# Kernel optimization log

Measured on AMD Instinct MI355X. Metric: run time of the kernel, lower is better.

Reference implementation:

```python
import jax, jax.numpy as jnp
import numpy as np

B, S, D, H = 4, 2048, 512, 4
HD = D // H
EPS = 1e-5


def layer_norm(x, gamma, beta):
    mu = jnp.mean(x, axis=-1, keepdims=True)
    var = jnp.mean(jnp.square(x - mu), axis=-1, keepdims=True)
    return (x - mu) * jax.lax.rsqrt(var + EPS) * gamma + beta


def setup_inputs() -> dict:
    key = jax.random.key(0)
    ks = jax.random.split(key, 16)
    s_in = 1.0 / np.sqrt(D)
    s_ex = 1.0 / np.sqrt(2 * D)
    return {
        "input_states": jax.random.normal(ks[0], (B, S, D), jnp.float32),
        "positions": jax.random.normal(ks[1], (B, S, 3), jnp.float32),
        "W_expand": jax.random.uniform(ks[2], (D, 2 * D), jnp.float32, -s_in, s_in),
        "b_expand": jax.random.uniform(ks[3], (2 * D,), jnp.float32, -s_in, s_in),
        "W_squeeze": jax.random.uniform(ks[4], (2 * D, D), jnp.float32, -s_ex, s_ex),
        "b_squeeze": jax.random.uniform(ks[5], (D,), jnp.float32, -s_ex, s_ex),
        "gamma": jnp.ones((D,), jnp.float32),
        "beta": jnp.zeros((D,), jnp.float32),
        "Wq": jax.random.uniform(ks[6], (D, D), jnp.float32, -s_in, s_in),
        "bq": jax.random.uniform(ks[7], (D,), jnp.float32, -s_in, s_in),
        "Wk": jax.random.uniform(ks[8], (D, D), jnp.float32, -s_in, s_in),
        "bk": jax.random.uniform(ks[9], (D,), jnp.float32, -s_in, s_in),
        "Wv": jax.random.uniform(ks[10], (D, D), jnp.float32, -s_in, s_in),
        "bv": jax.random.uniform(ks[11], (D,), jnp.float32, -s_in, s_in),
        "alpha": jnp.float32(0.1),
    }


def reference(input_states, positions, W_expand, b_expand, W_squeeze, b_squeeze,
              gamma, beta, Wq, bq, Wk, bk, Wv, bv, alpha):
    # FFN (expand -> relu -> squeeze) + residual + LayerNorm
    h = jax.nn.relu(input_states @ W_expand + b_expand)
    squeezed = h @ W_squeeze + b_squeeze
    se = layer_norm(input_states + squeezed, gamma, beta)

    # q/k/v projections, split heads: [B,H,S,HD]
    q = (se @ Wq + bq).reshape(B, S, H, HD).transpose(0, 2, 1, 3)
    k = (se @ Wk + bk).reshape(B, S, H, HD).transpose(0, 2, 1, 3)
    v = (se @ Wv + bv).reshape(B, S, H, HD).transpose(0, 2, 1, 3)

    scores = jnp.einsum('bhid,bhjd->bhij', q, k) / np.sqrt(HD)

    # squared pairwise distance bias: ||pi||^2 + ||pj||^2 - 2 pi.pj, broadcast over heads
    sq = jnp.sum(positions * positions, axis=-1)  # [B,S]
    dist2 = sq[:, :, None] + sq[:, None, :] - 2.0 * jnp.einsum('bic,bjc->bij', positions, positions)
    dist2 = jnp.maximum(dist2, 0.0)
    scores = scores - alpha * dist2[:, None, :, :]

    w = jax.nn.softmax(scores, axis=-1)
    ctx = jnp.einsum('bhij,bhjd->bhid', w, v)
    ctx = ctx.transpose(0, 2, 1, 3).reshape(B, S, D)

    # same LayerNorm params reused (self.norm applied twice in original)
    return layer_norm(se + ctx, gamma, beta)
```

## Files before the change

### kernel.cpp

```cpp
#include <hip/hip_runtime.h>

typedef __bf16 bf16_t;
typedef __attribute__((ext_vector_type(8))) __bf16 bf16x8;
typedef __attribute__((ext_vector_type(4))) __bf16 bf16x4;
typedef __attribute__((ext_vector_type(4))) float f32x4;

constexpr int Bc = 4, Sc = 2048, Dc = 512, Hc = 4, HDc = 128;
constexpr int Mrows = Bc * Sc;

__device__ inline void gl2lds(const void* g, void* l) {
  __builtin_amdgcn_global_load_lds(
      (__attribute__((address_space(1))) void*)g,
      (__attribute__((address_space(3))) void*)l, 16, 0, 0);
}

__global__ __launch_bounds__(256) void prep_k(
    const float* __restrict__ X, bf16_t* __restrict__ xb,
    const float* __restrict__ We, bf16_t* __restrict__ wtE,
    const float* __restrict__ Ws, bf16_t* __restrict__ wtS,
    const float* __restrict__ Wq, const float* __restrict__ Wk,
    const float* __restrict__ Wv, bf16_t* __restrict__ wtQKV) {
  const int bid = blockIdx.x;
  if (bid < 2048) {
    const long i = ((long)bid * 256 + threadIdx.x) * 8;
    const float4 a = *(const float4*)(X + i);
    const float4 c = *(const float4*)(X + i + 4);
    bf16x8 o;
    o[0] = (bf16_t)a.x; o[1] = (bf16_t)a.y; o[2] = (bf16_t)a.z; o[3] = (bf16_t)a.w;
    o[4] = (bf16_t)c.x; o[5] = (bf16_t)c.y; o[6] = (bf16_t)c.z; o[7] = (bf16_t)c.w;
    *(bf16x8*)(xb + i) = o;
    return;
  }
  __shared__ float tile[32][33];
  const float* src; bf16_t* dst; int K, N, local;
  if (bid < 2560)      { src = We; dst = wtE; K = 512;  N = 1024; local = bid - 2048; }
  else if (bid < 3072) { src = Ws; dst = wtS; K = 1024; N = 512;  local = bid - 2560; }
  else if (bid < 3328) { src = Wq; dst = wtQKV;          K = 512; N = 512; local = bid - 3072; }
  else if (bid < 3584) { src = Wk; dst = wtQKV + 262144; K = 512; N = 512; local = bid - 3328; }
  else                 { src = Wv; dst = wtQKV + 524288; K = 512; N = 512; local = bid - 3584; }
  const int nb = N / 32;
  const int n0 = (local % nb) * 32, k0 = (local / nb) * 32;
  const int tx = threadIdx.x & 31, ty = threadIdx.x >> 5;
#pragma unroll
  for (int i = 0; i < 4; i++)
    tile[ty + i * 8][tx] = src[(long)(k0 + ty + i * 8) * N + n0 + tx];
  __syncthreads();
#pragma unroll
  for (int i = 0; i < 4; i++)
    dst[(long)(n0 + ty + i * 8) * K + k0 + tx] = (bf16_t)tile[tx][ty + i * 8];
}

__global__ __launch_bounds__(256) void pospack_k(const float* __restrict__ pos,
                                                 const float* __restrict__ alphap,
                                                 float* __restrict__ pos2) {
  const float aL = alphap[0] * 1.4426950408889634f;
  const int i = blockIdx.x * 256 + threadIdx.x;
  const float x = pos[(long)i * 3], y = pos[(long)i * 3 + 1], z = pos[(long)i * 3 + 2];
  float4 o; o.x = x; o.y = y; o.z = z; o.w = -aL * (x * x + y * y + z * z);
  *(float4*)(pos2 + (long)i * 4) = o;
}

template <int OMODE>
__global__ __launch_bounds__(256, 3) void gemm128_k(
    const bf16_t* __restrict__ A, const bf16_t* __restrict__ Bt,
    const float* __restrict__ bias0, const float* __restrict__ bias1,
    const float* __restrict__ bias2, void* __restrict__ out0,
    void* __restrict__ out1, void* __restrict__ out2, int N, int K) {
  __shared__ bf16_t As[128 * 64];
  __shared__ bf16_t Bs[128 * 64];
  const int t = threadIdx.x;
  const int n0 = blockIdx.x * 128, m0 = blockIdx.y * 128;
  const int lane = t & 63, wave = t >> 6;
  const int quad = lane >> 4, ln = lane & 15;
  const int wm = wave >> 1, wn = wave & 1;
  const int srow = wave * 32 + (lane >> 3);
  const int sgrp = lane & 7;
  const bf16_t* aseg = A + (long)(m0 + srow) * K + sgrp * 8;
  const bf16_t* bseg = Bt + (long)(n0 + srow) * K + sgrp * 8;
  bf16_t* asl = &As[(wave * 32) * 64];
  bf16_t* bsl = &Bs[(wave * 32) * 64];
  f32x4 acc[4][4] = {};
  for (int k0 = 0; k0 < K; k0 += 64) {
#pragma unroll
    for (int i = 0; i < 4; i++) {
      gl2lds(aseg + (long)i * 8 * K + k0, asl + i * 8 * 64);
      gl2lds(bseg + (long)i * 8 * K + k0, bsl + i * 8 * 64);
    }
    __syncthreads();
#pragma unroll
    for (int kc = 0; kc < 2; kc++) {
      bf16x8 af[4], bfr[4];
#pragma unroll
      for (int mt = 0; mt < 4; mt++)
        af[mt] = *(const bf16x8*)&As[(wm * 64 + mt * 16 + ln) * 64 + kc * 32 + quad * 8];
#pragma unroll
      for (int nt = 0; nt < 4; nt++)
        bfr[nt] = *(const bf16x8*)&Bs[(wn * 64 + nt * 16 + ln) * 64 + kc * 32 + quad * 8];
#pragma unroll
      for (int mt = 0; mt < 4; mt++)
#pragma unroll
        for (int nt = 0; nt < 4; nt++)
          acc[mt][nt] = __builtin_amdgcn_mfma_f32_16x16x32_bf16(af[mt], bfr[nt],
                                                                acc[mt][nt], 0, 0, 0);
    }
    __syncthreads();
  }
#pragma unroll
  for (int nt = 0; nt < 4; nt++) {
    const int gcol = n0 + wn * 64 + nt * 16 + ln;
    if constexpr (OMODE == 0 || OMODE == 1) {
      const float bv = bias0[gcol];
      bf16_t* o = (bf16_t*)out0;
#pragma unroll
      for (int mt = 0; mt < 4; mt++)
#pragma unroll
        for (int r = 0; r < 4; r++) {
          const int grow = m0 + wm * 64 + mt * 16 + quad * 4 + r;
          float vv = acc[mt][nt][r] + bv;
          if constexpr (OMODE == 0) vv = vv > 0.f ? vv : 0.f;
          o[(long)grow * N + gcol] = (bf16_t)vv;
        }
    } else {
      const int which = gcol >> 9, n = gcol & 511;
      const int hh = n >> 7, hd = n & 127;
      const float bv = (which == 0 ? bias0 : which == 1 ? bias1 : bias2)[n];
      bf16_t* o = (bf16_t*)(which == 0 ? out0 : which == 1 ? out1 : out2);
#pragma unroll
      for (int mt = 0; mt < 4; mt++)
#pragma unroll
        for (int r = 0; r < 4; r++) {
          const int grow = m0 + wm * 64 + mt * 16 + quad * 4 + r;
          const int b = grow >> 11, s = grow & 2047;
          const float vv = acc[mt][nt][r] + bv;
          long idx;
          if (which == 2)
            idx = ((long)(b * Hc + hh) * HDc + hd) * Sc + s;
          else
            idx = ((long)(b * Hc + hh) * Sc + s) * HDc + hd;
          o[idx] = (bf16_t)vv;
        }
    }
  }
}

template <int DUAL>
__global__ __launch_bounds__(256) void ln_k(const float* __restrict__ xa,
                                            const bf16_t* __restrict__ xb,
                                            const float* __restrict__ gamma,
                                            const float* __restrict__ beta,
                                            float* __restrict__ out,
                                            bf16_t* __restrict__ outb) {
  const int wave = threadIdx.x >> 6, lane = threadIdx.x & 63;
  const long row = (long)blockIdx.x * 4 + wave;
  const float* a = xa + row * Dc;
  const bf16_t* bp = xb + row * Dc;
  float vv[8];
  float s = 0.f, s2 = 0.f;
#pragma unroll
  for (int i = 0; i < 2; i++) {
    const float4 va = *(const float4*)(a + lane * 4 + i * 256);
    const bf16x4 vb = *(const bf16x4*)(bp + lane * 4 + i * 256);
    const float xs[4] = {va.x, va.y, va.z, va.w};
#pragma unroll
    for (int j = 0; j < 4; j++) {
      const float x = xs[j] + (float)vb[j];
      vv[i * 4 + j] = x;
      s += x;
      s2 += x * x;
    }
  }
#pragma unroll
  for (int off = 1; off < 64; off <<= 1) {
    s += __shfl_xor(s, off, 64);
    s2 += __shfl_xor(s2, off, 64);
  }
  const float mu = s * (1.f / Dc);
  const float var = s2 * (1.f / Dc) - mu * mu;
  const float rstd = rsqrtf(var + 1e-5f);
#pragma unroll
  for (int i = 0; i < 2; i++)
#pragma unroll
    for (int j = 0; j < 4; j++) {
      const int col = lane * 4 + i * 256 + j;
      const float o = (vv[i * 4 + j] - mu) * rstd * gamma[col] + beta[col];
      out[row * Dc + col] = o;
      if constexpr (DUAL) outb[row * Dc + col] = (bf16_t)o;
    }
}

__global__ __launch_bounds__(256, 2) void attn_k(const bf16_t* __restrict__ q,
                                                 const bf16_t* __restrict__ k,
                                                 const bf16_t* __restrict__ v,
                                                 const float* __restrict__ pos2,
                                                 const float* __restrict__ alphap,
                                                 bf16_t* __restrict__ ctx) {
  __shared__ bf16_t Ks[2][64 * 128];
  __shared__ bf16_t Vts[2][128 * 64];
  __shared__ float pk[2][64][4];
  __shared__ bf16_t Ps[4][16][72];
  const int t = threadIdx.x;
  const int qt = blockIdx.x, h = blockIdx.y, b = blockIdx.z;
  const int q0 = qt * 64;
  const int wave = t >> 6, lane = t & 63, quad = lane >> 4, ln = lane & 15;
  const int ln7 = ln & 7;
  const float l2e = 1.4426950408889634f;
  const float scale_l2 = 0.08838834764831845f * l2e;
  const float aL2 = alphap[0] * l2e;
  const float twoaL = 2.f * aL2;
  const bf16_t* kbase = k + (long)(b * Hc + h) * Sc * HDc;
  const bf16_t* vbase = v + (long)(b * Hc + h) * HDc * Sc;

  bf16x8 qf[4];
#pragma unroll
  for (int kc = 0; kc < 4; kc++)
    qf[kc] = *(const bf16x8*)(q + ((long)(b * Hc + h) * Sc + q0 + wave * 16 + ln) * HDc +
                              kc * 32 + quad * 8);
  float pqx[4], pqy[4], pqz[4], pqw[4];
#pragma unroll
  for (int r = 0; r < 4; r++) {
    const float4 p = *(const float4*)(pos2 + ((long)b * Sc + q0 + wave * 16 + quad * 4 + r) * 4);
    pqx[r] = twoaL * p.x; pqy[r] = twoaL * p.y; pqz[r] = twoaL * p.z; pqw[r] = p.w;
  }

  const int krw = wave * 16 + (lane >> 4);
  const int kg = lane & 15;
  const int vrw = wave * 32 + (lane >> 3);
  const int vg = lane & 7;
  const bf16_t* kcur = kbase;
  const bf16_t* vcur = vbase;
  const float* pcur = pos2 + (long)b * Sc * 4;
  auto stage = [&](int buf) {
#pragma unroll
    for (int i = 0; i < 4; i++) {
      const int row = krw + i * 4;
      gl2lds(kcur + (long)row * HDc + (kg ^ (row & 7)) * 8, &Ks[buf][wave * 2048 + i * 512]);
    }
#pragma unroll
    for (int i = 0; i < 4; i++) {
      const int row = vrw + i * 8;
      gl2lds(vcur + (long)row * Sc + (vg ^ (row & 7)) * 8, &Vts[buf][wave * 2048 + i * 512]);
    }
    if (wave == 0) gl2lds(pcur, &pk[buf][0][0]);
  };
  stage(0);
  kcur += 64 * HDc; vcur += 64; pcur += 256;

  float rs[4] = {0.f, 0.f, 0.f, 0.f};
  f32x4 acc_o[8] = {};

  for (int kt = 0; kt < Sc / 64; kt++) {
    const int cur = kt & 1;
    __syncthreads();
    if (kt < Sc / 64 - 1) {
      stage(1 - cur);
      kcur += 64 * HDc; vcur += 64; pcur += 256;
    }

    f32x4 sacc[4] = {};
#pragma unroll
    for (int kc = 0; kc < 4; kc++)
#pragma unroll
      for (int ct = 0; ct < 4; ct++) {
        const bf16x8 bfv = *(const bf16x8*)&Ks[cur][(ct * 16 + ln) * 128 +
                                                    ((kc * 4 + quad) ^ ln7) * 8];
        sacc[ct] = __builtin_amdgcn_mfma_f32_16x16x32_bf16(qf[kc], bfv, sacc[ct], 0, 0, 0);
      }
#pragma unroll
    for (int ct = 0; ct < 4; ct++) {
      const int kk = ct * 16 + ln;
      const float4 pkv = *(const float4*)&pk[cur][kk][0];
#pragma unroll
      for (int r = 0; r < 4; r++) {
        float base = pqw[r] + pkv.w;
        base = __builtin_fmaf(pqx[r], pkv.x, base);
        base = __builtin_fmaf(pqy[r], pkv.y, base);
        base = __builtin_fmaf(pqz[r], pkv.z, base);
        const float p = __builtin_amdgcn_exp2f(__builtin_fmaf(sacc[ct][r], scale_l2, base));
        rs[r] += p;
        Ps[wave][quad * 4 + r][kk] = (bf16_t)p;
      }
    }
#pragma unroll
    for (int s2 = 0; s2 < 2; s2++) {
      const bf16x8 pf = *(const bf16x8*)&Ps[wave][ln][s2 * 32 + quad * 8];
#pragma unroll
      for (int nt = 0; nt < 8; nt++) {
        const bf16x8 vf = *(const bf16x8*)&Vts[cur][(nt * 16 + ln) * 64 +
                                                    ((s2 * 4 + quad) ^ ln7) * 8];
        acc_o[nt] = __builtin_amdgcn_mfma_f32_16x16x32_bf16(pf, vf, acc_o[nt], 0, 0, 0);
      }
    }
  }

#pragma unroll
  for (int off = 1; off < 16; off <<= 1)
#pragma unroll
    for (int r = 0; r < 4; r++) rs[r] += __shfl_xor(rs[r], off, 64);
  float rinv[4];
#pragma unroll
  for (int r = 0; r < 4; r++) rinv[r] = 1.f / rs[r];
#pragma unroll
  for (int nt = 0; nt < 8; nt++)
#pragma unroll
    for (int r = 0; r < 4; r++) {
      const int qrow = wave * 16 + quad * 4 + r;
      ctx[((long)b * Sc + q0 + qrow) * Dc + h * HDc + nt * 16 + ln] =
          (bf16_t)(acc_o[nt][r] * rinv[r]);
    }
}

constexpr size_t SE_OFF = 0;
constexpr size_t SQB_OFF = 16777216;
constexpr size_t SEB_OFF = 25165824;
constexpr size_t Q_OFF = 33554432;
constexpr size_t K_OFF = 41943040;
constexpr size_t V_OFF = 50331648;
constexpr size_t XB_OFF = Q_OFF;
constexpr size_t H_OFF = K_OFF;
constexpr size_t POS2_OFF = SEB_OFF;
constexpr size_t WTE_OFF = 58720256;
constexpr size_t WTS_OFF = WTE_OFF + 1048576;
constexpr size_t WTQKV_OFF = WTS_OFF + 1048576;

extern "C" void kernel_launch(void* const* d_in, const int* in_sizes, int n_in,
                              void* d_out, int out_size, void* d_ws, size_t ws_size,
                              hipStream_t stream) {
  const float* X = (const float*)d_in[0];
  const float* pos = (const float*)d_in[1];
  const float* W_expand = (const float*)d_in[2];
  const float* b_expand = (const float*)d_in[3];
  const float* W_squeeze = (const float*)d_in[4];
  const float* b_squeeze = (const float*)d_in[5];
  const float* gamma = (const float*)d_in[6];
  const float* beta = (const float*)d_in[7];
  const float* Wq = (const float*)d_in[8];
  const float* bq = (const float*)d_in[9];
  const float* Wk = (const float*)d_in[10];
  const float* bk = (const float*)d_in[11];
  const float* Wv = (const float*)d_in[12];
  const float* bv = (const float*)d_in[13];
  const float* alphap = (const float*)d_in[14];

  char* ws = (char*)d_ws;
  float* se = (float*)(ws + SE_OFF);
  bf16_t* sqb = (bf16_t*)(ws + SQB_OFF);
  bf16_t* ctxb = (bf16_t*)(ws + SQB_OFF);
  bf16_t* seb = (bf16_t*)(ws + SEB_OFF);
  float* pos2 = (float*)(ws + POS2_OFF);
  bf16_t* qb = (bf16_t*)(ws + Q_OFF);
  bf16_t* kb = (bf16_t*)(ws + K_OFF);
  bf16_t* vb = (bf16_t*)(ws + V_OFF);
  bf16_t* xbb = (bf16_t*)(ws + XB_OFF);
  bf16_t* hb = (bf16_t*)(ws + H_OFF);
  bf16_t* wtE = (bf16_t*)(ws + WTE_OFF);
  bf16_t* wtS = (bf16_t*)(ws + WTS_OFF);
  bf16_t* wtQKV = (bf16_t*)(ws + WTQKV_OFF);

  prep_k<<<3840, 256, 0, stream>>>(X, xbb, W_expand, wtE, W_squeeze, wtS,
                                   Wq, Wk, Wv, wtQKV);

  gemm128_k<0><<<dim3(1024 / 128, Mrows / 128), 256, 0, stream>>>(
      xbb, wtE, b_expand, nullptr, nullptr, hb, nullptr, nullptr, 1024, 512);
  gemm128_k<1><<<dim3(512 / 128, Mrows / 128), 256, 0, stream>>>(
      hb, wtS, b_squeeze, nullptr, nullptr, sqb, nullptr, nullptr, 512, 1024);
  ln_k<1><<<Mrows / 4, 256, 0, stream>>>(X, sqb, gamma, beta, se, seb);
  gemm128_k<2><<<dim3(1536 / 128, Mrows / 128), 256, 0, stream>>>(
      seb, wtQKV, bq, bk, bv, qb, kb, vb, 1536, 512);
  pospack_k<<<Mrows / 256, 256, 0, stream>>>(pos, alphap, pos2);
  attn_k<<<dim3(Sc / 64, Hc, Bc), 256, 0, stream>>>(qb, kb, vb, pos2, alphap, ctxb);
  ln_k<0><<<Mrows / 4, 256, 0, stream>>>(se, ctxb, gamma, beta, (float*)d_out, nullptr);

  (void)in_sizes; (void)n_in; (void)out_size; (void)ws_size;
}
```

Measured before the change: 243.4 us.

## Pre-tile K/V into MFMA fragment layout and switch attention to 32x32 MFMA with key split

The QKV GEMM epilogue now writes K and V in a pre-swizzled per-tile fragment order, so the attention kernel can stage them with contiguous global-to-LDS copies and read fragments with lane-linear LDS loads. Attention moves from 16x16x32 to 32x32x16 MFMA. Waves split the 64-key tile in halves over 32 query rows each, and the two partial outputs and row sums are combined through LDS at the end. Separately, the squeeze GEMM uses a 64-wide N tile so more blocks cover the device. The cost is scattered stores in the QKV epilogue and an extra LDS reduction pass in attention.

```diff
diff --git a/kernel.cpp b/kernel.cpp
--- a/kernel.cpp
+++ b/kernel.cpp
@@ -4,6 +4,7 @@
 typedef __attribute__((ext_vector_type(8))) __bf16 bf16x8;
 typedef __attribute__((ext_vector_type(4))) __bf16 bf16x4;
 typedef __attribute__((ext_vector_type(4))) float f32x4;
+typedef __attribute__((ext_vector_type(16))) float f32x16;
 
 constexpr int Bc = 4, Sc = 2048, Dc = 512, Hc = 4, HDc = 128;
 constexpr int Mrows = Bc * Sc;
@@ -60,44 +61,48 @@
   *(float4*)(pos2 + (long)i * 4) = o;
 }
 
-template <int OMODE>
+template <int OMODE, int TN>
 __global__ __launch_bounds__(256, 3) void gemm128_k(
     const bf16_t* __restrict__ A, const bf16_t* __restrict__ Bt,
     const float* __restrict__ bias0, const float* __restrict__ bias1,
     const float* __restrict__ bias2, void* __restrict__ out0,
     void* __restrict__ out1, void* __restrict__ out2, int N, int K) {
   __shared__ bf16_t As[128 * 64];
-  __shared__ bf16_t Bs[128 * 64];
+  __shared__ bf16_t Bs[TN * 64];
+  constexpr int MT = (TN == 128) ? 4 : 2;
+  constexpr int BI = (TN == 128) ? 4 : 2;
+  constexpr int MW = (TN == 128) ? 64 : 32;
   const int t = threadIdx.x;
-  const int n0 = blockIdx.x * 128, m0 = blockIdx.y * 128;
+  const int n0 = blockIdx.x * TN, m0 = blockIdx.y * 128;
   const int lane = t & 63, wave = t >> 6;
   const int quad = lane >> 4, ln = lane & 15;
-  const int wm = wave >> 1, wn = wave & 1;
-  const int srow = wave * 32 + (lane >> 3);
-  const int sgrp = lane & 7;
-  const bf16_t* aseg = A + (long)(m0 + srow) * K + sgrp * 8;
-  const bf16_t* bseg = Bt + (long)(n0 + srow) * K + sgrp * 8;
+  const int wm = (TN == 128) ? (wave >> 1) : wave;
+  const int wn = (TN == 128) ? (wave & 1) : 0;
+  const int l8 = lane >> 3, g = lane & 7;
+  const bf16_t* aseg = A + (long)(m0 + wave * 32 + l8) * K + g * 8;
+  const bf16_t* bseg = Bt + (long)(n0 + wave * (BI * 8) + l8) * K + g * 8;
   bf16_t* asl = &As[(wave * 32) * 64];
-  bf16_t* bsl = &Bs[(wave * 32) * 64];
-  f32x4 acc[4][4] = {};
+  bf16_t* bsl = &Bs[(wave * BI * 8) * 64];
+  f32x4 acc[MT][4] = {};
   for (int k0 = 0; k0 < K; k0 += 64) {
 #pragma unroll
-    for (int i = 0; i < 4; i++) {
+    for (int i = 0; i < 4; i++)
       gl2lds(aseg + (long)i * 8 * K + k0, asl + i * 8 * 64);
+#pragma unroll
+    for (int i = 0; i < BI; i++)
       gl2lds(bseg + (long)i * 8 * K + k0, bsl + i * 8 * 64);
-    }
     __syncthreads();
 #pragma unroll
     for (int kc = 0; kc < 2; kc++) {
-      bf16x8 af[4], bfr[4];
-#pragma unroll
-      for (int mt = 0; mt < 4; mt++)
-        af[mt] = *(const bf16x8*)&As[(wm * 64 + mt * 16 + ln) * 64 + kc * 32 + quad * 8];
+      bf16x8 af[MT], bfr[4];
+#pragma unroll
+      for (int mt = 0; mt < MT; mt++)
+        af[mt] = *(const bf16x8*)&As[(wm * MW + mt * 16 + ln) * 64 + kc * 32 + quad * 8];
 #pragma unroll
       for (int nt = 0; nt < 4; nt++)
         bfr[nt] = *(const bf16x8*)&Bs[(wn * 64 + nt * 16 + ln) * 64 + kc * 32 + quad * 8];
 #pragma unroll
-      for (int mt = 0; mt < 4; mt++)
+      for (int mt = 0; mt < MT; mt++)
 #pragma unroll
         for (int nt = 0; nt < 4; nt++)
           acc[mt][nt] = __builtin_amdgcn_mfma_f32_16x16x32_bf16(af[mt], bfr[nt],
@@ -112,10 +117,10 @@
       const float bv = bias0[gcol];
       bf16_t* o = (bf16_t*)out0;
 #pragma unroll
-      for (int mt = 0; mt < 4; mt++)
+      for (int mt = 0; mt < MT; mt++)
 #pragma unroll
         for (int r = 0; r < 4; r++) {
-          const int grow = m0 + wm * 64 + mt * 16 + quad * 4 + r;
+          const int grow = m0 + wm * MW + mt * 16 + quad * 4 + r;
           float vv = acc[mt][nt][r] + bv;
           if constexpr (OMODE == 0) vv = vv > 0.f ? vv : 0.f;
           o[(long)grow * N + gcol] = (bf16_t)vv;
@@ -126,17 +131,24 @@
       const float bv = (which == 0 ? bias0 : which == 1 ? bias1 : bias2)[n];
       bf16_t* o = (bf16_t*)(which == 0 ? out0 : which == 1 ? out1 : out2);
 #pragma unroll
-      for (int mt = 0; mt < 4; mt++)
+      for (int mt = 0; mt < MT; mt++)
 #pragma unroll
         for (int r = 0; r < 4; r++) {
-          const int grow = m0 + wm * 64 + mt * 16 + quad * 4 + r;
+          const int grow = m0 + wm * MW + mt * 16 + quad * 4 + r;
           const int b = grow >> 11, s = grow & 2047;
           const float vv = acc[mt][nt][r] + bv;
           long idx;
-          if (which == 2)
-            idx = ((long)(b * Hc + hh) * HDc + hd) * Sc + s;
-          else
-            idx = ((long)(b * Hc + hh) * Sc + s) * HDc + hd;
+          if (which == 0) {
+            idx = ((long)((b * Hc + hh) * Sc + s)) * HDc + hd;
+          } else if (which == 1) {
+            const int tt = s >> 6, kh = (s >> 5) & 1, key = s & 31;
+            const int c = hd >> 4, lk = key + 32 * ((hd >> 3) & 1), j = hd & 7;
+            idx = ((((long)((b * Hc + hh) * 32 + tt) * 2 + kh) * 8 + c) * 64 + lk) * 8 + j;
+          } else {
+            const int tt = s >> 6, ht2 = hd >> 5, kc = (s & 63) >> 4;
+            const int lk = (hd & 31) + 32 * ((s >> 3) & 1), j = s & 7;
+            idx = ((((long)((b * Hc + hh) * 32 + tt) * 4 + ht2) * 4 + kc) * 64 + lk) * 8 + j;
+          }
           o[idx] = (bf16_t)vv;
         }
     }
@@ -189,124 +201,125 @@
 }
 
 __global__ __launch_bounds__(256, 2) void attn_k(const bf16_t* __restrict__ q,
-                                                 const bf16_t* __restrict__ k,
-                                                 const bf16_t* __restrict__ v,
+                                                 const bf16_t* __restrict__ Kg,
+                                                 const bf16_t* __restrict__ Vg,
                                                  const float* __restrict__ pos2,
                                                  const float* __restrict__ alphap,
                                                  bf16_t* __restrict__ ctx) {
-  __shared__ bf16_t Ks[2][64 * 128];
-  __shared__ bf16_t Vts[2][128 * 64];
-  __shared__ float pk[2][64][4];
-  __shared__ bf16_t Ps[4][16][72];
+  __shared__ bf16_t Ks[2][8192];
+  __shared__ bf16_t Vts[2][8192];
+  __shared__ float pk4[2][64][4];
+  __shared__ bf16_t Ps[4][1024];
+  __shared__ float RsD[4][32];
   const int t = threadIdx.x;
   const int qt = blockIdx.x, h = blockIdx.y, b = blockIdx.z;
   const int q0 = qt * 64;
-  const int wave = t >> 6, lane = t & 63, quad = lane >> 4, ln = lane & 15;
-  const int ln7 = ln & 7;
+  const int wave = t >> 6, lane = t & 63;
+  const int l31 = lane & 31, hb = lane >> 5;
+  const int rh = wave & 1, kh = wave >> 1;
   const float l2e = 1.4426950408889634f;
-  const float scale_l2 = 0.08838834764831845f * l2e;
-  const float aL2 = alphap[0] * l2e;
-  const float twoaL = 2.f * aL2;
-  const bf16_t* kbase = k + (long)(b * Hc + h) * Sc * HDc;
-  const bf16_t* vbase = v + (long)(b * Hc + h) * HDc * Sc;
-
-  bf16x8 qf[4];
-#pragma unroll
-  for (int kc = 0; kc < 4; kc++)
-    qf[kc] = *(const bf16x8*)(q + ((long)(b * Hc + h) * Sc + q0 + wave * 16 + ln) * HDc +
-                              kc * 32 + quad * 8);
-  float pqx[4], pqy[4], pqz[4], pqw[4];
-#pragma unroll
-  for (int r = 0; r < 4; r++) {
-    const float4 p = *(const float4*)(pos2 + ((long)b * Sc + q0 + wave * 16 + quad * 4 + r) * 4);
-    pqx[r] = twoaL * p.x; pqy[r] = twoaL * p.y; pqz[r] = twoaL * p.z; pqw[r] = p.w;
-  }
-
-  const int krw = wave * 16 + (lane >> 4);
-  const int kg = lane & 15;
-  const int vrw = wave * 32 + (lane >> 3);
-  const int vg = lane & 7;
-  const bf16_t* kcur = kbase;
-  const bf16_t* vcur = vbase;
-  const float* pcur = pos2 + (long)b * Sc * 4;
+  const float scale_l2 = l2e * 0.08838834764831845f;
+  const float aL = alphap[0] * l2e;
+
+  bf16x8 qf[8];
+  const long qrow = (long)((b * Hc + h) * Sc + q0 + rh * 32 + l31);
+#pragma unroll
+  for (int c = 0; c < 8; c++)
+    qf[c] = *(const bf16x8*)(q + qrow * HDc + c * 16 + hb * 8);
+  float pqx, pqy, pqz;
+  {
+    const float4 p = *(const float4*)(pos2 + (long)(b * Sc + q0 + rh * 32 + l31) * 4);
+    pqx = 2.f * aL * p.x; pqy = 2.f * aL * p.y; pqz = 2.f * aL * p.z;
+  }
+
+  const bf16_t* ktile = Kg + (long)((b * Hc + h) * 32) * 8192 + lane * 8;
+  const bf16_t* vtile = Vg + (long)((b * Hc + h) * 32) * 8192 + lane * 8;
+  const float* pcur = pos2 + (long)b * Sc * 4 + lane * 4;
   auto stage = [&](int buf) {
 #pragma unroll
-    for (int i = 0; i < 4; i++) {
-      const int row = krw + i * 4;
-      gl2lds(kcur + (long)row * HDc + (kg ^ (row & 7)) * 8, &Ks[buf][wave * 2048 + i * 512]);
-    }
-#pragma unroll
-    for (int i = 0; i < 4; i++) {
-      const int row = vrw + i * 8;
-      gl2lds(vcur + (long)row * Sc + (vg ^ (row & 7)) * 8, &Vts[buf][wave * 2048 + i * 512]);
-    }
-    if (wave == 0) gl2lds(pcur, &pk[buf][0][0]);
+    for (int i = 0; i < 4; i++)
+      gl2lds(ktile + (wave * 4 + i) * 512, &Ks[buf][(wave * 4 + i) * 512]);
+#pragma unroll
+    for (int i = 0; i < 4; i++)
+      gl2lds(vtile + (wave * 4 + i) * 512, &Vts[buf][(wave * 4 + i) * 512]);
+    if (wave == 0) gl2lds(pcur, &pk4[buf][0][0]);
   };
   stage(0);
-  kcur += 64 * HDc; vcur += 64; pcur += 256;
-
-  float rs[4] = {0.f, 0.f, 0.f, 0.f};
-  f32x4 acc_o[8] = {};
+  ktile += 8192; vtile += 8192; pcur += 256;
+
+  float rsl = 0.f;
+  f32x16 accT[4] = {};
+  bf16_t* pwbase = &Ps[wave][l31 * 8 + 4 * hb];
 
   for (int kt = 0; kt < Sc / 64; kt++) {
     const int cur = kt & 1;
     __syncthreads();
     if (kt < Sc / 64 - 1) {
       stage(1 - cur);
-      kcur += 64 * HDc; vcur += 64; pcur += 256;
-    }
-
-    f32x4 sacc[4] = {};
-#pragma unroll
-    for (int kc = 0; kc < 4; kc++)
-#pragma unroll
-      for (int ct = 0; ct < 4; ct++) {
-        const bf16x8 bfv = *(const bf16x8*)&Ks[cur][(ct * 16 + ln) * 128 +
-                                                    ((kc * 4 + quad) ^ ln7) * 8];
-        sacc[ct] = __builtin_amdgcn_mfma_f32_16x16x32_bf16(qf[kc], bfv, sacc[ct], 0, 0, 0);
+      ktile += 8192; vtile += 8192; pcur += 256;
+    }
+    f32x16 sacc = {};
+#pragma unroll
+    for (int c = 0; c < 8; c++) {
+      const bf16x8 kf = *(const bf16x8*)&Ks[cur][(kh * 8 + c) * 512 + lane * 8];
+      sacc = __builtin_amdgcn_mfma_f32_32x32x16_bf16(kf, qf[c], sacc, 0, 0, 0);
+    }
+#pragma unroll
+    for (int g2 = 0; g2 < 4; g2++)
+#pragma unroll
+      for (int r0 = 0; r0 < 4; r0++) {
+        const int kp = r0 + 4 * hb + 8 * g2;
+        const float4 pv = *(const float4*)&pk4[cur][kh * 32 + kp][0];
+        const float bias = __builtin_fmaf(pqx, pv.x,
+                           __builtin_fmaf(pqy, pv.y,
+                           __builtin_fmaf(pqz, pv.z, pv.w)));
+        const float p = __builtin_amdgcn_exp2f(
+            __builtin_fmaf(sacc[g2 * 4 + r0], scale_l2, bias));
+        rsl += p;
+        pwbase[(g2 >> 1) * 512 + (g2 & 1) * 256 + r0] = (bf16_t)p;
       }
-#pragma unroll
-    for (int ct = 0; ct < 4; ct++) {
-      const int kk = ct * 16 + ln;
-      const float4 pkv = *(const float4*)&pk[cur][kk][0];
-#pragma unroll
-      for (int r = 0; r < 4; r++) {
-        float base = pqw[r] + pkv.w;
-        base = __builtin_fmaf(pqx[r], pkv.x, base);
-        base = __builtin_fmaf(pqy[r], pkv.y, base);
-        base = __builtin_fmaf(pqz[r], pkv.z, base);
-        const float p = __builtin_amdgcn_exp2f(__builtin_fmaf(sacc[ct][r], scale_l2, base));
-        rs[r] += p;
-        Ps[wave][quad * 4 + r][kk] = (bf16_t)p;
+    const bf16x8 pf0 = *(const bf16x8*)&Ps[wave][lane * 8];
+    const bf16x8 pf1 = *(const bf16x8*)&Ps[wave][512 + lane * 8];
+#pragma unroll
+    for (int ht = 0; ht < 4; ht++) {
+      const bf16x8 v0 = *(const bf16x8*)&Vts[cur][(ht * 4 + kh * 2 + 0) * 512 + lane * 8];
+      accT[ht] = __builtin_amdgcn_mfma_f32_32x32x16_bf16(v0, pf0, accT[ht], 0, 0, 0);
+      const bf16x8 v1 = *(const bf16x8*)&Vts[cur][(ht * 4 + kh * 2 + 1) * 512 + lane * 8];
+      accT[ht] = __builtin_amdgcn_mfma_f32_32x32x16_bf16(v1, pf1, accT[ht], 0, 0, 0);
+    }
+  }
+  __syncthreads();
+
+  rsl += __shfl_xor(rsl, 32, 64);
+  if (hb == 0) RsD[wave][l31] = rsl;
+  float* Oc = (float*)&Ks[0][0];
+  if (kh == 1) {
+#pragma unroll
+    for (int ht = 0; ht < 4; ht++)
+#pragma unroll
+      for (int r = 0; r < 16; r++) {
+        const int hdp = (r & 3) + 8 * (r >> 2) + 4 * hb;
+        Oc[(ht * 32 + hdp) * 64 + rh * 32 + l31] = accT[ht][r];
       }
-    }
-#pragma unroll
-    for (int s2 = 0; s2 < 2; s2++) {
-      const bf16x8 pf = *(const bf16x8*)&Ps[wave][ln][s2 * 32 + quad * 8];
-#pragma unroll
-      for (int nt = 0; nt < 8; nt++) {
-        const bf16x8 vf = *(const bf16x8*)&Vts[cur][(nt * 16 + ln) * 64 +
-                                                    ((s2 * 4 + quad) ^ ln7) * 8];
-        acc_o[nt] = __builtin_amdgcn_mfma_f32_16x16x32_bf16(pf, vf, acc_o[nt], 0, 0, 0);
+  }
+  __syncthreads();
+  if (kh == 0) {
+    const float rinv = 1.f / (RsD[wave][l31] + RsD[wave + 2][l31]);
+    const long orow = (long)(b * Sc + q0 + rh * 32 + l31);
+#pragma unroll
+    for (int ht = 0; ht < 4; ht++)
+#pragma unroll
+      for (int g2 = 0; g2 < 4; g2++) {
+        bf16x4 ov;
+#pragma unroll
+        for (int r0 = 0; r0 < 4; r0++) {
+          const int hdp = r0 + 8 * g2 + 4 * hb;
+          ov[r0] = (bf16_t)((accT[ht][g2 * 4 + r0] +
+                             Oc[(ht * 32 + hdp) * 64 + rh * 32 + l31]) * rinv);
+        }
+        *(bf16x4*)(ctx + orow * Dc + h * HDc + ht * 32 + 8 * g2 + 4 * hb) = ov;
       }
-    }
-  }
-
-#pragma unroll
-  for (int off = 1; off < 16; off <<= 1)
-#pragma unroll
-    for (int r = 0; r < 4; r++) rs[r] += __shfl_xor(rs[r], off, 64);
-  float rinv[4];
-#pragma unroll
-  for (int r = 0; r < 4; r++) rinv[r] = 1.f / rs[r];
-#pragma unroll
-  for (int nt = 0; nt < 8; nt++)
-#pragma unroll
-    for (int r = 0; r < 4; r++) {
-      const int qrow = wave * 16 + quad * 4 + r;
-      ctx[((long)b * Sc + q0 + qrow) * Dc + h * HDc + nt * 16 + ln] =
-          (bf16_t)(acc_o[nt][r] * rinv[r]);
-    }
+  }
 }
 
 constexpr size_t SE_OFF = 0;
@@ -358,13 +371,12 @@
 
   prep_k<<<3840, 256, 0, stream>>>(X, xbb, W_expand, wtE, W_squeeze, wtS,
                                    Wq, Wk, Wv, wtQKV);
-
-  gemm128_k<0><<<dim3(1024 / 128, Mrows / 128), 256, 0, stream>>>(
+  gemm128_k<0, 128><<<dim3(1024 / 128, Mrows / 128), 256, 0, stream>>>(
       xbb, wtE, b_expand, nullptr, nullptr, hb, nullptr, nullptr, 1024, 512);
-  gemm128_k<1><<<dim3(512 / 128, Mrows / 128), 256, 0, stream>>>(
+  gemm128_k<1, 64><<<dim3(512 / 64, Mrows / 128), 256, 0, stream>>>(
       hb, wtS, b_squeeze, nullptr, nullptr, sqb, nullptr, nullptr, 512, 1024);
   ln_k<1><<<Mrows / 4, 256, 0, stream>>>(X, sqb, gamma, beta, se, seb);
-  gemm128_k<2><<<dim3(1536 / 128, Mrows / 128), 256, 0, stream>>>(
+  gemm128_k<2, 128><<<dim3(1536 / 128, Mrows / 128), 256, 0, stream>>>(
       seb, wtQKV, bq, bk, bv, qb, kb, vb, 1536, 512);
   pospack_k<<<Mrows / 256, 256, 0, stream>>>(pos, alphap, pos2);
   attn_k<<<dim3(Sc / 64, Hc, Bc), 256, 0, stream>>>(qb, kb, vb, pos2, alphap, ctxb);
```

Result: faster. 235.7 us (-3.2%).
